# Kernel optimization log

Hardware: AMD Instinct MI355X
Metric: run time of the kernel (lower is better)

The kernel has to match this reference:

```python
import jax, jax.numpy as jnp
import numpy as np

N, F_IN, HID, HEADS, NCLS, E = 50000, 512, 64, 4, 64, 800000
NEG_SLOPE = 0.2
EPS = 1e-16


def setup_inputs() -> dict:
    key = jax.random.key(0)
    ks = jax.random.split(key, 10)
    s = 0.1
    return {
        "x": jax.random.normal(ks[0], (N, F_IN), jnp.float32),
        "edge_index": jax.random.randint(ks[1], (2, E), 0, N, jnp.int64),
        "W1": jax.random.normal(ks[2], (F_IN, HEADS * HID), jnp.float32) * s,
        "a_src1": jax.random.normal(ks[3], (HEADS, HID), jnp.float32) * s,
        "a_dst1": jax.random.normal(ks[4], (HEADS, HID), jnp.float32) * s,
        "b1": jax.random.normal(ks[5], (HEADS * HID,), jnp.float32) * s,
        "W2": jax.random.normal(ks[6], (HEADS * HID, NCLS), jnp.float32) * s,
        "a_src2": jax.random.normal(ks[7], (1, NCLS), jnp.float32) * s,
        "a_dst2": jax.random.normal(ks[8], (1, NCLS), jnp.float32) * s,
        "b2": jax.random.normal(ks[9], (NCLS,), jnp.float32) * s,
    }


def gat_conv(x, W, a_src, a_dst, b, src, dst):
    H, C = a_src.shape
    h = (x @ W).reshape(-1, H, C)                     # [N, H, C]
    # per-node attention halves, gathered per edge -> [E', H]
    al_src = jnp.einsum("nhc,hc->nh", h, a_src)
    al_dst = jnp.einsum("nhc,hc->nh", h, a_dst)
    e = jax.nn.leaky_relu(al_src[src] + al_dst[dst], NEG_SLOPE)
    # segment softmax over destination neighborhoods
    m = jax.ops.segment_max(e, dst, num_segments=x.shape[0])
    ex = jnp.exp(e - m[dst])
    denom = jax.ops.segment_sum(ex, dst, num_segments=x.shape[0])
    alpha = ex / (denom[dst] + EPS)                   # [E', H]
    out = jax.ops.segment_sum(alpha[:, :, None] * h[src], dst,
                              num_segments=x.shape[0])  # [N, H, C]
    return out.reshape(-1, H * C) + b


def reference(x, edge_index, W1, a_src1, a_dst1, b1, W2, a_src2, a_dst2, b2):
    n = x.shape[0]
    loop = jnp.arange(n, dtype=edge_index.dtype)
    src = jnp.concatenate([edge_index[0], loop])       # add self loops (PyG default)
    dst = jnp.concatenate([edge_index[1], loop])
    h = gat_conv(x, W1, a_src1, a_dst1, b1, src, dst)
    h = jax.nn.elu(h)                                  # dropout is identity in eval
    out = gat_conv(h, W2, a_src2, a_dst2, b2, src, dst)
    return jax.nn.log_softmax(out, axis=1)
```

## Files before the change

### kernel.cpp

```cpp
#include <hip/hip_runtime.h>
#include <math.h>

#define F_IN 512
#define HC1 256
#define HEADS 4
#define HID 64
#define NCLS 64
#define NEG_SLOPE 0.2f
#define EPS_DENOM 1e-16f

using short8 = __attribute__((ext_vector_type(8))) short;
using f32x4  = __attribute__((ext_vector_type(4))) float;

__device__ inline float wave_sum(float v) {
#pragma unroll
  for (int s = 32; s > 0; s >>= 1) v += __shfl_xor(v, s);
  return v;
}

__device__ inline unsigned short f2bf(float f) {
  unsigned int u = __float_as_uint(f);
  u = (u + 0x7FFF + ((u >> 16) & 1)) >> 16;
  return (unsigned short)u;
}
__device__ inline float bflo(unsigned int u) { return __uint_as_float(u << 16); }
__device__ inline float bfhi(unsigned int u) { return __uint_as_float(u & 0xFFFF0000u); }

__device__ inline unsigned int cvtpk_bf16(float lo, float hi) {
  unsigned int r;
  asm("v_cvt_pk_bf16_f32 %0, %1, %2" : "=v"(r) : "v"(lo), "v"(hi));
  return r;
}

__device__ inline void async_copy16(const void* g, void* l) {
  __builtin_amdgcn_global_load_lds((const __attribute__((address_space(1))) void*)g,
                                   (__attribute__((address_space(3))) void*)l, 16, 0, 0);
}

__global__ void castT_kernel(const float* __restrict__ W, unsigned short* __restrict__ WT,
                             int K, int Nn) {
  int id = blockIdx.x * blockDim.x + threadIdx.x;
  if (id >= K * Nn) return;
  int n = id / K, k = id % K;
  WT[id] = f2bf(W[(size_t)k * Nn + n]);
}


__global__ void hist_kernel(const int* __restrict__ dst, int E, int* __restrict__ cnt) {
  int i = blockIdx.x * blockDim.x + threadIdx.x;
  int stride = gridDim.x * blockDim.x;
  for (int e = i; e < E; e += stride) atomicAdd(&cnt[dst[e]], 1);
}

__global__ void scan_blocks_kernel(const int* __restrict__ cnt, int n,
                                   int* __restrict__ rowoff, int* __restrict__ cursor,
                                   int* __restrict__ bsum) {
  __shared__ int wpart[16];
  int b = blockIdx.x, tid = threadIdx.x;
  int i = b * 1024 + tid;
  int lane = tid & 63, wid = tid >> 6;
  int v = (i < n) ? (cnt[i] + 1) : 0;
  int x = v;
#pragma unroll
  for (int s = 1; s < 64; s <<= 1) {
    int t = __shfl_up(x, s);
    if (lane >= s) x += t;
  }
  if (lane == 63) wpart[wid] = x;
  __syncthreads();
  if (wid == 0) {
    int p = (lane < 16) ? wpart[lane] : 0;
#pragma unroll
    for (int s = 1; s < 16; s <<= 1) {
      int t = __shfl_up(p, s);
      if (lane >= s) p += t;
    }
    if (lane < 16) wpart[lane] = p;
  }
  __syncthreads();
  int incl = x + (wid ? wpart[wid - 1] : 0);
  if (i < n) { rowoff[i + 1] = incl; cursor[i] = incl - v; }
  if (tid == 1023) bsum[b] = incl;
  if (b == 0 && tid == 0) rowoff[0] = 0;
}

__global__ void scan_partials_kernel(int* __restrict__ bsum, int nb) {
  int lane = threadIdx.x;
  int v = (lane < nb) ? bsum[lane] : 0;
  int x = v;
#pragma unroll
  for (int s = 1; s < 64; s <<= 1) {
    int t = __shfl_up(x, s);
    if (lane >= s) x += t;
  }
  if (lane < nb) bsum[lane] = x - v;
}

__global__ void scan_add_kernel(int n, int* __restrict__ rowoff, int* __restrict__ cursor,
                                const int* __restrict__ bsum) {
  int i = blockIdx.x * 1024 + threadIdx.x;
  int off = bsum[blockIdx.x];
  if (i < n) { rowoff[i + 1] += off; cursor[i] += off; }
}

__global__ void scatter_kernel(const int* __restrict__ src, const int* __restrict__ dst,
                               int E, int n, int* __restrict__ cursor, int* __restrict__ esrc) {
  int i = blockIdx.x * blockDim.x + threadIdx.x;
  int stride = gridDim.x * blockDim.x;
  for (int e = i; e < E + n; e += stride) {
    int s, d;
    if (e < E) { s = src[e]; d = dst[e]; } else { s = e - E; d = s; }
    int pos = atomicAdd(&cursor[d], 1);
    esrc[pos] = s;
  }
}


__global__ __launch_bounds__(256)
void gemm1_fused_kernel(const float* __restrict__ A, const unsigned short* __restrict__ BT,
                        unsigned short* __restrict__ Cb,
                        const float* __restrict__ as1, const float* __restrict__ ad1,
                        float* __restrict__ als, float* __restrict__ ald, int M) {
  constexpr int BM = 64, BN = 256, BK = 32, K = F_IN, Nn = HC1;
  __shared__ float          Af[2][BM * BK];
  __shared__ unsigned short Bh[2][BN * BK];
  const int t = threadIdx.x;
  const int lane = t & 63;
  const int w = t >> 6;
  const int wc = w * 64;
  const int row0 = blockIdx.x * BM;
  const int lrow = lane & 15;
  const int lkf = (lane >> 4) * 8;

  auto stageA = [&](int buf, int k0) {
#pragma unroll
    for (int i = 0; i < 2; ++i) {
      int c = i * 256 + t;
      int r = c >> 3, slot = c & 7;
      int grow = row0 + r; if (grow > M - 1) grow = M - 1;
      const float* g = A + (size_t)grow * K + k0 + ((slot ^ (r & 7)) << 2);
      async_copy16(g, (char*)&Af[buf][0] + (size_t)(i * 256 + w * 64) * 16);
    }
  };
  auto stageB = [&](int buf, int k0) {
#pragma unroll
    for (int i = 0; i < 4; ++i) {
      int c = i * 256 + t;
      int r = c >> 2, slot = c & 3;
      const unsigned short* g = BT + (size_t)r * K + k0 + ((slot ^ (r & 3)) << 3);
      async_copy16(g, (char*)&Bh[buf][0] + (size_t)(i * 256 + w * 64) * 16);
    }
  };

  f32x4 acc[4][4] = {};
  stageA(0, 0); stageB(0, 0);
  int cur = 0;
  for (int k0 = 0; k0 < K; k0 += BK) {
    __syncthreads();
    if (k0 + BK < K) { stageA(cur ^ 1, k0 + BK); stageB(cur ^ 1, k0 + BK); }
    short8 a[4], b[4];
#pragma unroll
    for (int m = 0; m < 4; ++m) {
      int r = m * 16 + lrow;
      int s0 = lkf >> 2;
      const char* base = (const char*)&Af[cur][0] + (size_t)r * 128;
      float4 f0 = *(const float4*)(base + (((s0    ) ^ (r & 7)) << 4));
      float4 f1 = *(const float4*)(base + (((s0 | 1) ^ (r & 7)) << 4));
      union { short8 s; uint4 u; } pk;
      pk.u.x = cvtpk_bf16(f0.x, f0.y); pk.u.y = cvtpk_bf16(f0.z, f0.w);
      pk.u.z = cvtpk_bf16(f1.x, f1.y); pk.u.w = cvtpk_bf16(f1.z, f1.w);
      a[m] = pk.s;
    }
#pragma unroll
    for (int n = 0; n < 4; ++n) {
      int r = wc + n * 16 + lrow;
      int slot = lkf >> 3;
      b[n] = *(const short8*)((const char*)&Bh[cur][0] + (size_t)r * 64 +
                              (((slot ^ (r & 3))) << 4));
    }
#pragma unroll
    for (int m = 0; m < 4; ++m)
#pragma unroll
      for (int n = 0; n < 4; ++n)
        acc[m][n] = __builtin_amdgcn_mfma_f32_16x16x32_bf16(a[m], b[n], acc[m][n], 0, 0, 0);
    cur ^= 1;
  }

  float asv[4], adv[4];
#pragma unroll
  for (int n = 0; n < 4; ++n) {
    asv[n] = as1[w * 64 + n * 16 + lrow];
    adv[n] = ad1[w * 64 + n * 16 + lrow];
  }
#pragma unroll
  for (int m = 0; m < 4; ++m) {
#pragma unroll
    for (int j = 0; j < 4; ++j) {
      int r = row0 + m * 16 + (lane >> 4) * 4 + j;
      float ps = 0.f, pd = 0.f;
#pragma unroll
      for (int n = 0; n < 4; ++n) {
        float v = acc[m][n][j];
        ps += v * asv[n];
        pd += v * adv[n];
        if (r < M) Cb[(size_t)r * Nn + wc + n * 16 + lrow] = f2bf(v);
      }
#pragma unroll
      for (int s = 1; s < 16; s <<= 1) {
        ps += __shfl_xor(ps, s);
        pd += __shfl_xor(pd, s);
      }
      if ((lane & 15) == 0 && r < M) {
        als[r * HEADS + w] = ps;
        ald[r * HEADS + w] = pd;
      }
    }
  }
}


__global__ __launch_bounds__(256)
void gemm2_fused_kernel(const unsigned short* __restrict__ A,
                        const unsigned short* __restrict__ BT,
                        unsigned short* __restrict__ Cb,
                        const float* __restrict__ as2, const float* __restrict__ ad2,
                        float* __restrict__ als, float* __restrict__ ald, int M) {
  constexpr int BM = 128, BN = 64, BK = 32, K = HC1, Nn = NCLS;
  __shared__ unsigned short Alds[BM * BK];
  __shared__ unsigned short Blds[BN * BK];
  __shared__ float sps[BM], spd[BM];
  const int t = threadIdx.x;
  const int lane = t & 63;
  const int w = t >> 6;
  const int wr = (w >> 1) * 64;
  const int wc = (w & 1) * 32;
  const int row0 = blockIdx.x * BM;
  const int lrow = lane & 15;
  const int lk = (lane >> 4) * 8;
  if (t < BM) { sps[t] = 0.f; spd[t] = 0.f; }

  f32x4 acc[4][2] = {};
  for (int k0 = 0; k0 < K; k0 += BK) {
#pragma unroll
    for (int i = 0; i < 2; ++i) {
      int c = i * 256 + t;
      int arr = c >> 2;
      int ak = (c & 3) * 8;
      int grow = row0 + arr; if (grow > M - 1) grow = M - 1;
      const unsigned short* g = A + (size_t)grow * K + k0 + ak;
      unsigned short* l = Alds + (size_t)(i * 256 + w * 64) * 8;
      async_copy16(g, l);
    }
    {
      int c = t;
      int br = c >> 2;
      int bk = (c & 3) * 8;
      const unsigned short* g = BT + (size_t)br * K + k0 + bk;
      unsigned short* l = Blds + (size_t)(w * 64) * 8;
      async_copy16(g, l);
    }
    __syncthreads();
    short8 a[4], b[2];
#pragma unroll
    for (int m = 0; m < 4; ++m)
      a[m] = *(const short8*)&Alds[(wr + m * 16 + lrow) * BK + lk];
#pragma unroll
    for (int n = 0; n < 2; ++n)
      b[n] = *(const short8*)&Blds[(wc + n * 16 + lrow) * BK + lk];
#pragma unroll
    for (int m = 0; m < 4; ++m)
#pragma unroll
      for (int n = 0; n < 2; ++n)
        acc[m][n] = __builtin_amdgcn_mfma_f32_16x16x32_bf16(a[m], b[n], acc[m][n], 0, 0, 0);
    __syncthreads();
  }

  float asv[2], adv[2];
#pragma unroll
  for (int n = 0; n < 2; ++n) {
    asv[n] = as2[wc + n * 16 + lrow];
    adv[n] = ad2[wc + n * 16 + lrow];
  }
#pragma unroll
  for (int m = 0; m < 4; ++m) {
#pragma unroll
    for (int j = 0; j < 4; ++j) {
      int rl = wr + m * 16 + (lane >> 4) * 4 + j;
      int r = row0 + rl;
      float ps = 0.f, pd = 0.f;
#pragma unroll
      for (int n = 0; n < 2; ++n) {
        float v = acc[m][n][j];
        ps += v * asv[n];
        pd += v * adv[n];
        if (r < M) Cb[(size_t)r * Nn + wc + n * 16 + lrow] = f2bf(v);
      }
#pragma unroll
      for (int s = 1; s < 16; s <<= 1) {
        ps += __shfl_xor(ps, s);
        pd += __shfl_xor(pd, s);
      }
      if ((lane & 15) == 0) {
        atomicAdd(&sps[rl], ps);
        atomicAdd(&spd[rl], pd);
      }
    }
  }
  __syncthreads();
  if (t < BM) {
    int r = row0 + t;
    if (r < M) { als[r] = sps[t]; ald[r] = spd[t]; }
  }
}


__global__ void agg1_kernel(const unsigned short* __restrict__ h1b,
                            const float4* __restrict__ als1, const float4* __restrict__ ald1,
                            const int* __restrict__ rowoff, const int* __restrict__ esrc,
                            const float* __restrict__ b1, unsigned short* __restrict__ hact,
                            int n) {
  __shared__ float wlds[4][256];
  __shared__ int   slds[4][64];
  int w = threadIdx.x >> 6;
  int node = blockIdx.x * 4 + w;
  if (node >= n) return;
  int lane = threadIdx.x & 63;
  int hi = lane >> 5;
  int cl = lane & 31;
  int head = cl >> 3;
  int beg = rowoff[node], end = rowoff[node + 1];
  float4 aldn = ald1[node];
  f32x4 accA = {0.f, 0.f, 0.f, 0.f};
  f32x4 accB = {0.f, 0.f, 0.f, 0.f};
  float dl0 = 0.f, dl1 = 0.f, dl2 = 0.f, dl3 = 0.f;

  for (int base = beg; base < end; base += 64) {
    int cnt = min(64, end - base);
    if (lane < cnt) {
      int s = esrc[base + lane];
      float4 av = als1[s];
      float v, w0, w1, w2, w3;
      v = av.x + aldn.x; v = fmaxf(v, NEG_SLOPE * v); w0 = __expf(v);
      v = av.y + aldn.y; v = fmaxf(v, NEG_SLOPE * v); w1 = __expf(v);
      v = av.z + aldn.z; v = fmaxf(v, NEG_SLOPE * v); w2 = __expf(v);
      v = av.w + aldn.w; v = fmaxf(v, NEG_SLOPE * v); w3 = __expf(v);
      dl0 += w0; dl1 += w1; dl2 += w2; dl3 += w3;
      slds[w][lane] = s;
      float4 wv = {w0, w1, w2, w3};
      *(float4*)&wlds[w][lane * 4] = wv;
    }

    uint4 dA[4], dB[4];
    float wA[4], wB[4];
    auto ISSUE = [&](int j0, uint4* d, float* wj) {
#pragma unroll
      for (int ii = 0; ii < 4; ++ii) {
        int e = j0 + 2 * ii + hi;
        bool val = e < cnt;
        int se = val ? e : 0;
        int ss = slds[w][se];
        wj[ii] = val ? wlds[w][se * 4 + head] : 0.f;
        d[ii] = *(const uint4*)&h1b[(size_t)ss * HC1 + cl * 8];
      }
    };
    auto CONSUME = [&](const uint4* d, const float* wj) {
#pragma unroll
      for (int ii = 0; ii < 4; ++ii) {
        float q = wj[ii];
        accA[0] += q * bflo(d[ii].x); accA[1] += q * bfhi(d[ii].x);
        accA[2] += q * bflo(d[ii].y); accA[3] += q * bfhi(d[ii].y);
        accB[0] += q * bflo(d[ii].z); accB[1] += q * bfhi(d[ii].z);
        accB[2] += q * bflo(d[ii].w); accB[3] += q * bfhi(d[ii].w);
      }
    };

    ISSUE(0, dA, wA);
    for (int j0 = 8;; j0 += 16) {
      bool hasB = j0 < cnt;
      if (hasB) ISSUE(j0, dB, wB);
      CONSUME(dA, wA);
      if (!hasB) break;
      bool hasA = (j0 + 8) < cnt;
      if (hasA) ISSUE(j0 + 8, dA, wA);
      CONSUME(dB, wB);
      if (!hasA) break;
    }
  }

#pragma unroll
  for (int k = 0; k < 4; ++k) {
    accA[k] += __shfl_xor(accA[k], 32);
    accB[k] += __shfl_xor(accB[k], 32);
  }
  float d0 = wave_sum(dl0), d1 = wave_sum(dl1);
  float d2 = wave_sum(dl2), d3 = wave_sum(dl3);
  float den = head < 2 ? (head == 0 ? d0 : d1) : (head == 2 ? d2 : d3);
  float rden = 1.f / (den + EPS_DENOM);
  if (hi == 0) {
    float4 bv0 = *(const float4*)&b1[cl * 8];
    float4 bv1 = *(const float4*)&b1[cl * 8 + 4];
    float o[8];
    o[0] = accA[0] * rden + bv0.x; o[1] = accA[1] * rden + bv0.y;
    o[2] = accA[2] * rden + bv0.z; o[3] = accA[3] * rden + bv0.w;
    o[4] = accB[0] * rden + bv1.x; o[5] = accB[1] * rden + bv1.y;
    o[6] = accB[2] * rden + bv1.z; o[7] = accB[3] * rden + bv1.w;
    ushort4 ov0, ov1;
#pragma unroll
    for (int k = 0; k < 8; ++k) o[k] = o[k] > 0.f ? o[k] : __expf(o[k]) - 1.f;
    ov0.x = f2bf(o[0]); ov0.y = f2bf(o[1]); ov0.z = f2bf(o[2]); ov0.w = f2bf(o[3]);
    ov1.x = f2bf(o[4]); ov1.y = f2bf(o[5]); ov1.z = f2bf(o[6]); ov1.w = f2bf(o[7]);
    *(ushort4*)&hact[(size_t)node * HC1 + cl * 8] = ov0;
    *(ushort4*)&hact[(size_t)node * HC1 + cl * 8 + 4] = ov1;
  }
}

__global__ void agg2_kernel(const unsigned short* __restrict__ h2b,
                            const float* __restrict__ als2, const float* __restrict__ ald2,
                            const int* __restrict__ rowoff, const int* __restrict__ esrc,
                            const float* __restrict__ b2, float* __restrict__ out, int n) {
  __shared__ float wlds[4][64];
  __shared__ int   slds[4][64];
  int w = threadIdx.x >> 6;
  int node = blockIdx.x * 4 + w;
  if (node >= n) return;
  int lane = threadIdx.x & 63;
  int eg = lane >> 3;
  int cl = lane & 7;
  int beg = rowoff[node], end = rowoff[node + 1];
  float aldn = ald2[node];
  f32x4 accA = {0.f, 0.f, 0.f, 0.f};
  f32x4 accB = {0.f, 0.f, 0.f, 0.f};
  float dl = 0.f;
  for (int base = beg; base < end; base += 64) {
    int cnt = min(64, end - base);
    if (lane < cnt) {
      int s = esrc[base + lane];
      float v = als2[s] + aldn;
      v = fmaxf(v, NEG_SLOPE * v);
      float wl = __expf(v);
      dl += wl;
      slds[w][lane] = s;
      wlds[w][lane] = wl;
    }
    for (int j0 = 0; j0 < cnt; j0 += 32) {
      uint4 d[4]; float wj[4];
#pragma unroll
      for (int ii = 0; ii < 4; ++ii) {
        int e = j0 + ii * 8 + eg;
        bool val = e < cnt;
        int se = val ? e : 0;
        int ss = slds[w][se];
        wj[ii] = val ? wlds[w][se] : 0.f;
        d[ii] = *(const uint4*)&h2b[(size_t)ss * NCLS + cl * 8];
      }
#pragma unroll
      for (int ii = 0; ii < 4; ++ii) {
        float q = wj[ii];
        accA[0] += q * bflo(d[ii].x); accA[1] += q * bfhi(d[ii].x);
        accA[2] += q * bflo(d[ii].y); accA[3] += q * bfhi(d[ii].y);
        accB[0] += q * bflo(d[ii].z); accB[1] += q * bfhi(d[ii].z);
        accB[2] += q * bflo(d[ii].w); accB[3] += q * bfhi(d[ii].w);
      }
    }
  }
#pragma unroll
  for (int s = 8; s < 64; s <<= 1) {
#pragma unroll
    for (int k = 0; k < 4; ++k) {
      accA[k] += __shfl_xor(accA[k], s);
      accB[k] += __shfl_xor(accB[k], s);
    }
  }
  float den = wave_sum(dl);
  float rden = 1.f / (den + EPS_DENOM);
  float4 bv0 = *(const float4*)&b2[cl * 8];
  float4 bv1 = *(const float4*)&b2[cl * 8 + 4];
  float o[8];
  o[0] = accA[0] * rden + bv0.x; o[1] = accA[1] * rden + bv0.y;
  o[2] = accA[2] * rden + bv0.z; o[3] = accA[3] * rden + bv0.w;
  o[4] = accB[0] * rden + bv1.x; o[5] = accB[1] * rden + bv1.y;
  o[6] = accB[2] * rden + bv1.z; o[7] = accB[3] * rden + bv1.w;
  float mx = o[0];
#pragma unroll
  for (int k = 1; k < 8; ++k) mx = fmaxf(mx, o[k]);
#pragma unroll
  for (int s = 1; s < 8; s <<= 1) mx = fmaxf(mx, __shfl_xor(mx, s));
  float sm = 0.f;
#pragma unroll
  for (int k = 0; k < 8; ++k) sm += __expf(o[k] - mx);
#pragma unroll
  for (int s = 1; s < 8; s <<= 1) sm += __shfl_xor(sm, s);
  float ls = mx + __logf(sm);
  if (lane < 8) {
    float4 q0 = {o[0] - ls, o[1] - ls, o[2] - ls, o[3] - ls};
    float4 q1 = {o[4] - ls, o[5] - ls, o[6] - ls, o[7] - ls};
    *(float4*)&out[(size_t)node * NCLS + cl * 8] = q0;
    *(float4*)&out[(size_t)node * NCLS + cl * 8 + 4] = q1;
  }
}


extern "C" void kernel_launch(void* const* d_in, const int* in_sizes, int n_in,
                              void* d_out, int out_size, void* d_ws, size_t ws_size,
                              hipStream_t stream) {
  const float* x      = (const float*)d_in[0];
  const int*   eidx   = (const int*)d_in[1];
  const float* W1     = (const float*)d_in[2];
  const float* a_src1 = (const float*)d_in[3];
  const float* a_dst1 = (const float*)d_in[4];
  const float* b1     = (const float*)d_in[5];
  const float* W2     = (const float*)d_in[6];
  const float* a_src2 = (const float*)d_in[7];
  const float* a_dst2 = (const float*)d_in[8];
  const float* b2     = (const float*)d_in[9];
  float* out = (float*)d_out;

  const int Nn = in_sizes[0] / F_IN;
  const int E  = in_sizes[1] / 2;
  const int* esrc_in = eidx;
  const int* edst_in = eidx + E;

  char* ws = (char*)d_ws;
  size_t off = 0;
  auto alloc = [&](size_t bytes) -> void* {
    void* p = ws + off;
    off += (bytes + 255) & ~(size_t)255;
    return p;
  };
  unsigned short* h1b    = (unsigned short*)alloc((size_t)Nn * HC1 * sizeof(short));
  unsigned short* hact   = (unsigned short*)alloc((size_t)Nn * HC1 * sizeof(short));
  unsigned short* h2b    = (unsigned short*)alloc((size_t)Nn * NCLS * sizeof(short));
  unsigned short* W1T    = (unsigned short*)alloc((size_t)F_IN * HC1 * sizeof(short));
  unsigned short* W2T    = (unsigned short*)alloc((size_t)HC1 * NCLS * sizeof(short));
  float*          als1   = (float*)alloc((size_t)Nn * HEADS * sizeof(float));
  float*          ald1   = (float*)alloc((size_t)Nn * HEADS * sizeof(float));
  float*          als2   = (float*)alloc((size_t)Nn * sizeof(float));
  float*          ald2   = (float*)alloc((size_t)Nn * sizeof(float));
  int*            cnt    = (int*)alloc((size_t)Nn * sizeof(int));
  int*            rowoff = (int*)alloc((size_t)(Nn + 1) * sizeof(int));
  int*            cursor = (int*)alloc((size_t)Nn * sizeof(int));
  int*            bsum   = (int*)alloc(256 * sizeof(int));
  int*            esrc   = (int*)alloc((size_t)(E + Nn) * sizeof(int));

  const int nscan = (Nn + 1023) / 1024;

  castT_kernel<<<(F_IN * HC1 + 255) / 256, 256, 0, stream>>>(W1, W1T, F_IN, HC1);
  castT_kernel<<<(HC1 * NCLS + 255) / 256, 256, 0, stream>>>(W2, W2T, HC1, NCLS);

  hipMemsetAsync(cnt, 0, (size_t)Nn * sizeof(int), stream);
  hist_kernel<<<(E + 255) / 256, 256, 0, stream>>>(edst_in, E, cnt);
  scan_blocks_kernel<<<nscan, 1024, 0, stream>>>(cnt, Nn, rowoff, cursor, bsum);
  scan_partials_kernel<<<1, 64, 0, stream>>>(bsum, nscan);
  scan_add_kernel<<<nscan, 1024, 0, stream>>>(Nn, rowoff, cursor, bsum);
  scatter_kernel<<<(E + Nn + 255) / 256, 256, 0, stream>>>(esrc_in, edst_in, E, Nn, cursor, esrc);

  {
    int blocks = (Nn + 63) / 64;
    gemm1_fused_kernel<<<blocks, 256, 0, stream>>>(x, W1T, h1b, a_src1, a_dst1,
                                                   als1, ald1, Nn);
    int ablocks = (Nn + 3) / 4;
    agg1_kernel<<<ablocks, 256, 0, stream>>>(h1b, (const float4*)als1, (const float4*)ald1,
                                             rowoff, esrc, b1, hact, Nn);
  }

  {
    int blocks = (Nn + 127) / 128;
    gemm2_fused_kernel<<<blocks, 256, 0, stream>>>(hact, W2T, h2b, a_src2, a_dst2,
                                                   als2, ald2, Nn);
    int ablocks = (Nn + 3) / 4;
    agg2_kernel<<<ablocks, 256, 0, stream>>>(h2b, als2, ald2, rowoff, esrc, b2, out, Nn);
  }
}
```

Before: 266.5 us.

## Merge prep launches, fold partial scan into add, retile gemm1 to 2D grid

```diff
diff --git a/kernel.cpp b/kernel.cpp
--- a/kernel.cpp
+++ b/kernel.cpp
@@ -37,12 +37,23 @@
                                    (__attribute__((address_space(3))) void*)l, 16, 0, 0);
 }
 
-__global__ void castT_kernel(const float* __restrict__ W, unsigned short* __restrict__ WT,
-                             int K, int Nn) {
+
+__global__ void prep_kernel(const float* __restrict__ W1, unsigned short* __restrict__ W1T,
+                            const float* __restrict__ W2, unsigned short* __restrict__ W2T,
+                            int* __restrict__ cnt, int n) {
+  const int n1 = F_IN * HC1;
+  const int n2 = HC1 * NCLS;
   int id = blockIdx.x * blockDim.x + threadIdx.x;
-  if (id >= K * Nn) return;
-  int n = id / K, k = id % K;
-  WT[id] = f2bf(W[(size_t)k * Nn + n]);
+  if (id < n1) {
+    int nn = id / F_IN, k = id % F_IN;
+    W1T[id] = f2bf(W1[(size_t)k * HC1 + nn]);
+  } else if (id < n1 + n2) {
+    int j = id - n1;
+    int nn = j / HC1, k = j % HC1;
+    W2T[j] = f2bf(W2[(size_t)k * NCLS + nn]);
+  } else if (id < n1 + n2 + n) {
+    cnt[id - n1 - n2] = 0;
+  }
 }
 
 
@@ -84,22 +95,23 @@
   if (b == 0 && tid == 0) rowoff[0] = 0;
 }
 
-__global__ void scan_partials_kernel(int* __restrict__ bsum, int nb) {
-  int lane = threadIdx.x;
-  int v = (lane < nb) ? bsum[lane] : 0;
-  int x = v;
-#pragma unroll
-  for (int s = 1; s < 64; s <<= 1) {
-    int t = __shfl_up(x, s);
-    if (lane >= s) x += t;
-  }
-  if (lane < nb) bsum[lane] = x - v;
-}
-
 __global__ void scan_add_kernel(int n, int* __restrict__ rowoff, int* __restrict__ cursor,
-                                const int* __restrict__ bsum) {
-  int i = blockIdx.x * 1024 + threadIdx.x;
-  int off = bsum[blockIdx.x];
+                                const int* __restrict__ bsum, int nb) {
+  __shared__ int sscan[64];
+  int tid = threadIdx.x;
+  if (tid < 64) {
+    int v = (tid < nb) ? bsum[tid] : 0;
+    int x = v;
+#pragma unroll
+    for (int s = 1; s < 64; s <<= 1) {
+      int t = __shfl_up(x, s);
+      if (tid >= s) x += t;
+    }
+    sscan[tid] = x;
+  }
+  __syncthreads();
+  int off = blockIdx.x ? sscan[blockIdx.x - 1] : 0;
+  int i = blockIdx.x * 1024 + tid;
   if (i < n) { rowoff[i + 1] += off; cursor[i] += off; }
 }
 
@@ -121,65 +133,62 @@
                         unsigned short* __restrict__ Cb,
                         const float* __restrict__ as1, const float* __restrict__ ad1,
                         float* __restrict__ als, float* __restrict__ ald, int M) {
-  constexpr int BM = 64, BN = 256, BK = 32, K = F_IN, Nn = HC1;
+  constexpr int BM = 64, BN = 128, BK = 32, K = F_IN, Nn = HC1;
   __shared__ float          Af[2][BM * BK];
   __shared__ unsigned short Bh[2][BN * BK];
   const int t = threadIdx.x;
   const int lane = t & 63;
   const int w = t >> 6;
-  const int wc = w * 64;
-  const int row0 = blockIdx.x * BM;
+  const int wrow = (w >> 1) * 32;
+  const int wcol = (w & 1) * 64;
+  const int row0 = blockIdx.y * BM;
+  const int col0 = blockIdx.x * BN;
+  const int head = (col0 + wcol) >> 6;
   const int lrow = lane & 15;
-  const int lkf = (lane >> 4) * 8;
+  const int lk = (lane >> 4) * 8;
 
   auto stageA = [&](int buf, int k0) {
 #pragma unroll
     for (int i = 0; i < 2; ++i) {
       int c = i * 256 + t;
-      int r = c >> 3, slot = c & 7;
+      int r = c >> 3, sl = c & 7;
       int grow = row0 + r; if (grow > M - 1) grow = M - 1;
-      const float* g = A + (size_t)grow * K + k0 + ((slot ^ (r & 7)) << 2);
+      const float* g = A + (size_t)grow * K + k0 + sl * 4;
       async_copy16(g, (char*)&Af[buf][0] + (size_t)(i * 256 + w * 64) * 16);
     }
   };
   auto stageB = [&](int buf, int k0) {
 #pragma unroll
-    for (int i = 0; i < 4; ++i) {
+    for (int i = 0; i < 2; ++i) {
       int c = i * 256 + t;
-      int r = c >> 2, slot = c & 3;
-      const unsigned short* g = BT + (size_t)r * K + k0 + ((slot ^ (r & 3)) << 3);
+      int r = c >> 2, sl = c & 3;
+      const unsigned short* g = BT + (size_t)(col0 + r) * K + k0 + sl * 8;
       async_copy16(g, (char*)&Bh[buf][0] + (size_t)(i * 256 + w * 64) * 16);
     }
   };
 
-  f32x4 acc[4][4] = {};
+  f32x4 acc[2][4] = {};
   stageA(0, 0); stageB(0, 0);
   int cur = 0;
   for (int k0 = 0; k0 < K; k0 += BK) {
     __syncthreads();
     if (k0 + BK < K) { stageA(cur ^ 1, k0 + BK); stageB(cur ^ 1, k0 + BK); }
-    short8 a[4], b[4];
-#pragma unroll
-    for (int m = 0; m < 4; ++m) {
-      int r = m * 16 + lrow;
-      int s0 = lkf >> 2;
-      const char* base = (const char*)&Af[cur][0] + (size_t)r * 128;
-      float4 f0 = *(const float4*)(base + (((s0    ) ^ (r & 7)) << 4));
-      float4 f1 = *(const float4*)(base + (((s0 | 1) ^ (r & 7)) << 4));
+    short8 a[2], b[4];
+#pragma unroll
+    for (int m = 0; m < 2; ++m) {
+      const float* base = &Af[cur][(wrow + m * 16 + lrow) * BK + lk];
+      float4 f0 = *(const float4*)base;
+      float4 f1 = *(const float4*)(base + 4);
       union { short8 s; uint4 u; } pk;
       pk.u.x = cvtpk_bf16(f0.x, f0.y); pk.u.y = cvtpk_bf16(f0.z, f0.w);
       pk.u.z = cvtpk_bf16(f1.x, f1.y); pk.u.w = cvtpk_bf16(f1.z, f1.w);
       a[m] = pk.s;
     }
 #pragma unroll
-    for (int n = 0; n < 4; ++n) {
-      int r = wc + n * 16 + lrow;
-      int slot = lkf >> 3;
-      b[n] = *(const short8*)((const char*)&Bh[cur][0] + (size_t)r * 64 +
-                              (((slot ^ (r & 3))) << 4));
-    }
-#pragma unroll
-    for (int m = 0; m < 4; ++m)
+    for (int n = 0; n < 4; ++n)
+      b[n] = *(const short8*)&Bh[cur][(wcol + n * 16 + lrow) * BK + lk];
+#pragma unroll
+    for (int m = 0; m < 2; ++m)
 #pragma unroll
       for (int n = 0; n < 4; ++n)
         acc[m][n] = __builtin_amdgcn_mfma_f32_16x16x32_bf16(a[m], b[n], acc[m][n], 0, 0, 0);
@@ -189,21 +198,21 @@
   float asv[4], adv[4];
 #pragma unroll
   for (int n = 0; n < 4; ++n) {
-    asv[n] = as1[w * 64 + n * 16 + lrow];
-    adv[n] = ad1[w * 64 + n * 16 + lrow];
-  }
-#pragma unroll
-  for (int m = 0; m < 4; ++m) {
+    asv[n] = as1[head * 64 + n * 16 + lrow];
+    adv[n] = ad1[head * 64 + n * 16 + lrow];
+  }
+#pragma unroll
+  for (int m = 0; m < 2; ++m) {
 #pragma unroll
     for (int j = 0; j < 4; ++j) {
-      int r = row0 + m * 16 + (lane >> 4) * 4 + j;
+      int r = row0 + wrow + m * 16 + (lane >> 4) * 4 + j;
       float ps = 0.f, pd = 0.f;
 #pragma unroll
       for (int n = 0; n < 4; ++n) {
         float v = acc[m][n][j];
         ps += v * asv[n];
         pd += v * adv[n];
-        if (r < M) Cb[(size_t)r * Nn + wc + n * 16 + lrow] = f2bf(v);
+        if (r < M) Cb[(size_t)r * Nn + col0 + wcol + n * 16 + lrow] = f2bf(v);
       }
 #pragma unroll
       for (int s = 1; s < 16; s <<= 1) {
@@ -211,8 +220,8 @@
         pd += __shfl_xor(pd, s);
       }
       if ((lane & 15) == 0 && r < M) {
-        als[r * HEADS + w] = ps;
-        ald[r * HEADS + w] = pd;
+        als[r * HEADS + head] = ps;
+        ald[r * HEADS + head] = pd;
       }
     }
   }
@@ -544,20 +553,19 @@
 
   const int nscan = (Nn + 1023) / 1024;
 
-  castT_kernel<<<(F_IN * HC1 + 255) / 256, 256, 0, stream>>>(W1, W1T, F_IN, HC1);
-  castT_kernel<<<(HC1 * NCLS + 255) / 256, 256, 0, stream>>>(W2, W2T, HC1, NCLS);
-
-  hipMemsetAsync(cnt, 0, (size_t)Nn * sizeof(int), stream);
+  {
+    int total = F_IN * HC1 + HC1 * NCLS + Nn;
+    prep_kernel<<<(total + 255) / 256, 256, 0, stream>>>(W1, W1T, W2, W2T, cnt, Nn);
+  }
   hist_kernel<<<(E + 255) / 256, 256, 0, stream>>>(edst_in, E, cnt);
   scan_blocks_kernel<<<nscan, 1024, 0, stream>>>(cnt, Nn, rowoff, cursor, bsum);
-  scan_partials_kernel<<<1, 64, 0, stream>>>(bsum, nscan);
-  scan_add_kernel<<<nscan, 1024, 0, stream>>>(Nn, rowoff, cursor, bsum);
+  scan_add_kernel<<<nscan, 1024, 0, stream>>>(Nn, rowoff, cursor, bsum, nscan);
   scatter_kernel<<<(E + Nn + 255) / 256, 256, 0, stream>>>(esrc_in, edst_in, E, Nn, cursor, esrc);
 
   {
-    int blocks = (Nn + 63) / 64;
-    gemm1_fused_kernel<<<blocks, 256, 0, stream>>>(x, W1T, h1b, a_src1, a_dst1,
-                                                   als1, ald1, Nn);
+    dim3 g(HC1 / 128, (Nn + 63) / 64);
+    gemm1_fused_kernel<<<g, 256, 0, stream>>>(x, W1T, h1b, a_src1, a_dst1,
+                                              als1, ald1, Nn);
     int ablocks = (Nn + 3) / 4;
     agg1_kernel<<<ablocks, 256, 0, stream>>>(h1b, (const float4*)als1, (const float4*)ald1,
                                              rowoff, esrc, b1, hact, Nn);
```

Measured after the change: 257.6 us. 3.3% less time.
